# Kernel optimization log

Hardware: AMD Instinct MI355X
Metric: run time of the kernel (lower is better)

The kernel has to match this reference:

```python
import jax, jax.numpy as jnp
import numpy as np

B, N_IN, N_LATENT, STEPS = 256, 1024, 128, 256


def setup_inputs() -> dict:
    key = jax.random.key(0)
    kx, kf, kt = jax.random.split(key, 3)
    x = jax.random.normal(kx, (B, N_IN), dtype=jnp.float32)
    # transform ~ N(0, 0.1) per module's initialize_weights
    transform = 0.1 * jax.random.normal(kf, (N_IN, N_LATENT), dtype=jnp.float32)
    # transition scaled so spectral radius ~0.9 (std*sqrt(n_latent) ~ 0.9)
    # to keep the 256-step linear recurrence numerically stable
    transition = (0.9 / np.sqrt(N_LATENT)) * jax.random.normal(
        kt, (N_LATENT, N_LATENT), dtype=jnp.float32)
    return {"x": x, "transform": transform, "transition": transition,
            "steps": STEPS}


def reference(x, transform, transition, steps):
    # x: [B, n_in] -> latent0: [B, n_latent]
    latent0 = x @ transform

    def step(lat, _):
        lat = lat @ transition  # [B, n_latent]
        return lat, lat

    # lats: [steps, B, n_latent] -- latent states AFTER each transition
    _, lats = jax.lax.scan(step, latent0, None, length=steps)
    # project all latent states back to data space in one contraction
    # out[b, n, s] = sum_l lats[s, b, l] * transform[n, l]
    out = jnp.einsum('sbl,nl->bns', lats, transform)  # [B, n_in, steps]
    return out
```

## Files before the change

### kernel.cpp

```cpp
#include <hip/hip_runtime.h>
#include <hip/hip_bf16.h>

#define NIN 1024
#define NL 128
#define CMS 32768
#define MAGIC 0x4D474331

typedef __attribute__((ext_vector_type(8))) short bf16x8_t;
typedef __attribute__((ext_vector_type(4))) float f32x4_t;

__device__ inline unsigned short f2bf(float f) {
    __hip_bfloat16 h = __float2bfloat16(f);
    return *reinterpret_cast<unsigned short*>(&h);
}
__device__ inline float bf2f(unsigned short u) {
    unsigned int x = (unsigned int)u << 16;
    return __uint_as_float(x);
}
__device__ inline ushort4 pack4(f32x4_t v) {
    ushort4 o;
    o.x = f2bf(v[0]); o.y = f2bf(v[1]); o.z = f2bf(v[2]); o.w = f2bf(v[3]);
    return o;
}

__device__ __forceinline__ void stageBT(const float* __restrict__ Bg,
                                        unsigned short* BtHi, unsigned short* BtLo) {
    int t = threadIdx.x;
    for (int idx = t; idx < 4096; idx += 256) {
        int l = idx >> 5, c4 = (idx & 31) * 4;
        f32x4_t v = *(const f32x4_t*)&Bg[(size_t)l * 128 + c4];
#pragma unroll
        for (int q = 0; q < 4; ++q) {
            int c = c4 + q;
            float f = v[q];
            unsigned short hi = f2bf(f);
            unsigned short lo = f2bf(f - bf2f(hi));
            int byt = c * 256 + ((2 * l) ^ ((c & 7) << 4));
            *(unsigned short*)((char*)BtHi + byt) = hi;
            *(unsigned short*)((char*)BtLo + byt) = lo;
        }
    }
}

__device__ __forceinline__ void stageBT_T(const float* __restrict__ Btr,
                                          unsigned short* BtHi, unsigned short* BtLo) {
    int t = threadIdx.x;
    for (int idx = t; idx < 4096; idx += 256) {
        int c = idx >> 5, l4 = (idx & 31) * 4;
        f32x4_t v = *(const f32x4_t*)&Btr[(size_t)c * 128 + l4];
        ushort4 hi, lo;
        hi.x = f2bf(v[0]); lo.x = f2bf(v[0] - bf2f(hi.x));
        hi.y = f2bf(v[1]); lo.y = f2bf(v[1] - bf2f(hi.y));
        hi.z = f2bf(v[2]); lo.z = f2bf(v[2] - bf2f(hi.z));
        hi.w = f2bf(v[3]); lo.w = f2bf(v[3] - bf2f(hi.w));
        int byt = c * 256 + ((2 * l4) ^ ((c & 7) << 4));
        *(ushort4*)((char*)BtHi + byt) = hi;
        *(ushort4*)((char*)BtLo + byt) = lo;
    }
}

__device__ __forceinline__ void loadX(const float* __restrict__ Ag, float* X) {
    int t = threadIdx.x;
    for (int idx = t; idx < 1024; idx += 256) {
        int rr = idx >> 5, c4 = (idx & 31) * 4;
        f32x4_t v = *(const f32x4_t*)&Ag[(size_t)rr * 128 + c4];
        *(f32x4_t*)((char*)X + rr * 512 + ((c4 * 4) ^ ((rr & 7) << 4))) = v;
    }
}

__device__ __forceinline__ void chainStage(const float* X, float* Xn,
                                           const unsigned short* BtHi,
                                           const unsigned short* BtLo) {
    int t = threadIdx.x, w = t >> 6, lane = t & 63;
    int r = lane & 15, g = lane >> 4;
    int rt = w & 1, ctb = (w >> 1) * 4;
    int rr = rt * 16 + r;
    int sw = (rr & 7) << 4;
    bf16x8_t avHi[4], avLo[4];
#pragma unroll
    for (int kk = 0; kk < 4; ++kk) {
        int c0 = (kk * 4 + g) * 8;
        f32x4_t x0 = *(const f32x4_t*)((const char*)X + rr * 512 + ((c0 * 4) ^ sw));
        f32x4_t x1 = *(const f32x4_t*)((const char*)X + rr * 512 + (((c0 + 4) * 4) ^ sw));
        bf16x8_t hi, lo;
#pragma unroll
        for (int q = 0; q < 4; ++q) {
            unsigned short h0 = f2bf(x0[q]);
            hi[q] = (short)h0;
            lo[q] = (short)f2bf(x0[q] - bf2f(h0));
            unsigned short h1 = f2bf(x1[q]);
            hi[4 + q] = (short)h1;
            lo[4 + q] = (short)f2bf(x1[q] - bf2f(h1));
        }
        avHi[kk] = hi; avLo[kk] = lo;
    }
#pragma unroll
    for (int ct = 0; ct < 4; ++ct) {
        int cb = (ctb + ct) * 16 + r;
        int swb = (cb & 7) << 4;
        f32x4_t acc = (f32x4_t){0.f, 0.f, 0.f, 0.f};
#pragma unroll
        for (int kk = 0; kk < 4; ++kk) {
            int lb2 = (kk * 4 + g) * 16;
            int byt = cb * 256 + (lb2 ^ swb);
            bf16x8_t bh = *(const bf16x8_t*)((const char*)BtHi + byt);
            bf16x8_t bl = *(const bf16x8_t*)((const char*)BtLo + byt);
            acc = __builtin_amdgcn_mfma_f32_16x16x32_bf16(bh, avHi[kk], acc, 0, 0, 0);
            acc = __builtin_amdgcn_mfma_f32_16x16x32_bf16(bh, avLo[kk], acc, 0, 0, 0);
            acc = __builtin_amdgcn_mfma_f32_16x16x32_bf16(bl, avHi[kk], acc, 0, 0, 0);
        }
        int cc = (ctb + ct) * 16 + g * 4;
        *(f32x4_t*)((char*)Xn + rr * 512 + ((cc * 4) ^ sw)) = acc;
    }
}

__device__ __forceinline__ void writeXf(const float* X, float* __restrict__ Df) {
    int t = threadIdx.x;
    for (int idx = t; idx < 1024; idx += 256) {
        int rr = idx >> 5, c4 = (idx & 31) * 4;
        f32x4_t v = *(const f32x4_t*)((const char*)X + rr * 512 + ((c4 * 4) ^ ((rr & 7) << 4)));
        *(f32x4_t*)&Df[(size_t)rr * 128 + c4] = v;
    }
}

__device__ __forceinline__ void writeXbf(const float* X,
                                         unsigned short* __restrict__ base, int rstride) {
    int t = threadIdx.x;
    for (int idx = t; idx < 1024; idx += 256) {
        int rr = idx >> 5, c4 = (idx & 31) * 4;
        f32x4_t v = *(const f32x4_t*)((const char*)X + rr * 512 + ((c4 * 4) ^ ((rr & 7) << 4)));
        *(ushort4*)&base[(size_t)rr * rstride + c4] = pack4(v);
    }
}

__device__ __forceinline__ void signal(int* cells, int ci) {
    __syncthreads();
    if (threadIdx.x == 0)
        __hip_atomic_store(&cells[ci], MAGIC, __ATOMIC_RELEASE,
                           __HIP_MEMORY_SCOPE_AGENT);
}
__device__ __forceinline__ void waitRange(int* cells, int c0, int n) {
    for (int q = 0; q < n; ++q) {
        for (int it = 0; it < (1 << 22); ++it) {
            if (__hip_atomic_load(&cells[c0 + q], __ATOMIC_ACQUIRE,
                                  __HIP_MEMORY_SCOPE_AGENT) == MAGIC)
                break;
            __builtin_amdgcn_s_sleep(2);
        }
    }
}

__global__ __launch_bounds__(256) void k_pre(const float* __restrict__ x,
                                             const float* __restrict__ tf,
                                             const float* __restrict__ tr,
                                             float* __restrict__ T4f,
                                             float* __restrict__ T16f,
                                             float* __restrict__ T32f,
                                             float* __restrict__ Cf,
                                             float* __restrict__ Cf1,
                                             unsigned short* __restrict__ Cc,
                                             unsigned short* __restrict__ H,
                                             int* __restrict__ cells) {
    __shared__ __align__(16) char lds[98304];
    unsigned short* BtHi = (unsigned short*)lds;
    unsigned short* BtLo = (unsigned short*)(lds + 32768);
    float* X0 = (float*)(lds + 65536);
    float* X1 = (float*)(lds + 65536 + 16384);
    int blk = blockIdx.x, t = threadIdx.x;

    if (blk < 32) {
        float* xr = (float*)lds;
        int b0 = blk * 8;
        for (int idx = t; idx < 2048; idx += 256) {
            int rr = idx >> 8, c = idx & 255;
            ((float4*)xr)[rr * 256 + c] =
                ((const float4*)(x + (size_t)(b0 + rr) * NIN))[c];
        }
        __syncthreads();
        int cg = t & 31, rs = t >> 5;
        const float* xp = xr + rs * NIN;
        f32x4_t acc = (f32x4_t){0.f, 0.f, 0.f, 0.f};
#pragma unroll 8
        for (int i = 0; i < NIN; ++i) {
            f32x4_t tv = *(const f32x4_t*)&tf[i * NL + cg * 4];
            acc += xp[i] * tv;
        }
        int row = b0 + rs;
        *(f32x4_t*)&Cf[(size_t)row * NL + cg * 4] = acc;
        *(ushort4*)&Cc[(size_t)row * NL + cg * 4] = pack4(acc);
        signal(cells, blk);
    } else if (blk < 36) {
        int r0 = (blk - 32) * 32;
        stageBT(tr, BtHi, BtLo);
        loadX(tr + (size_t)r0 * NL, X0);
        __syncthreads();
        float* cur = X0; float* nxt = X1;
        for (int s = 0; s < 3; ++s) {
            chainStage(cur, nxt, BtHi, BtLo);
            __syncthreads();
            float* tmp = cur; cur = nxt; nxt = tmp;
        }
        writeXf(cur, T4f + (size_t)r0 * NL);
        signal(cells, blk);
    } else if (blk < 40) {
        int i = blk - 36, r0 = i * 32;
        if (t == 0) { waitRange(cells, 32, 4); __threadfence(); }
        __syncthreads();
        stageBT(T4f, BtHi, BtLo);
        loadX(T4f + (size_t)r0 * NL, X0);
        __syncthreads();
        float* cur = X0; float* nxt = X1;
        for (int s = 1; s <= 7; ++s) {
            chainStage(cur, nxt, BtHi, BtLo);
            __syncthreads();
            if (s == 3) {
                writeXf(nxt, T16f + (size_t)r0 * NL);
                signal(cells, 36 + i);
            }
            if (s == 7) {
                writeXf(nxt, T32f + (size_t)r0 * NL);
                signal(cells, 40 + i);
            }
            float* tmp = cur; cur = nxt; nxt = tmp;
        }
    } else if (blk < 48) {
        int cb = blk - 40, r0 = cb * 32;
        if (t == 0) {
            waitRange(cells, 36, 4);
            waitRange(cells, cb * 4, 4);
            __threadfence();
        }
        __syncthreads();
        stageBT(T16f, BtHi, BtLo);
        loadX(Cf + (size_t)r0 * NL, X0);
        __syncthreads();
        chainStage(X0, X1, BtHi, BtLo);
        __syncthreads();
        writeXf(X1, Cf1 + (size_t)r0 * NL);
        writeXbf(X1, Cc + (size_t)CMS + (size_t)r0 * NL, NL);
        signal(cells, 44 + cb);
    } else if (blk < 56) {
        int cb = blk - 48, r0 = cb * 32;
        if (t == 0) {
            waitRange(cells, 40, 4);
            waitRange(cells, cb * 4, 4);
            __threadfence();
        }
        __syncthreads();
        stageBT(T32f, BtHi, BtLo);
        loadX(Cf + (size_t)r0 * NL, X0);
        __syncthreads();
        float* cur = X0; float* nxt = X1;
        for (int k = 1; k <= 7; ++k) {
            chainStage(cur, nxt, BtHi, BtLo);
            __syncthreads();
            writeXbf(nxt, Cc + (size_t)(2 * k) * CMS + (size_t)r0 * NL, NL);
            float* tmp = cur; cur = nxt; nxt = tmp;
        }
    } else if (blk < 64) {
        int cb = blk - 56, r0 = cb * 32;
        if (t == 0) {
            waitRange(cells, 40, 4);
            waitRange(cells, 44 + cb, 1);
            __threadfence();
        }
        __syncthreads();
        stageBT(T32f, BtHi, BtLo);
        loadX(Cf1 + (size_t)r0 * NL, X0);
        __syncthreads();
        float* cur = X0; float* nxt = X1;
        for (int k = 1; k <= 7; ++k) {
            chainStage(cur, nxt, BtHi, BtLo);
            __syncthreads();
            writeXbf(nxt, Cc + (size_t)(1 + 2 * k) * CMS + (size_t)r0 * NL, NL);
            float* tmp = cur; cur = nxt; nxt = tmp;
        }
    } else {
        int n0 = (blk - 64) * 32;
        stageBT_T(tr, BtHi, BtLo);
        loadX(tf + (size_t)n0 * NL, X0);
        __syncthreads();
        float* cur = X0; float* nxt = X1;
        for (int s = 1; s <= 16; ++s) {
            chainStage(cur, nxt, BtHi, BtLo);
            __syncthreads();
            writeXbf(nxt, H + ((size_t)n0 * 16 + (s - 1)) * NL, 16 * NL);
            float* tmp = cur; cur = nxt; nxt = tmp;
        }
    }
}

__global__ __launch_bounds__(256) void k_main(const unsigned short* __restrict__ Cc,
                                              const unsigned short* __restrict__ H,
                                              float* __restrict__ out) {
    int bid = blockIdx.x;
    int e = ((bid & 7) << 7) | (bid >> 3);
    int ct = e >> 3, bt = (e >> 2) & 1, jq = e & 3;
    __shared__ __align__(16) char lds[49152];
    char* lB = lds;
    int t = threadIdx.x;
    const unsigned short* Bg = H + (size_t)(ct * 128) * NL;
    for (int i = t; i < 2048; i += 256) {
        int row = i >> 4, c = i & 15;
        int sw = (c * 16) ^ ((row & 7) << 4);
        *(bf16x8_t*)(lB + row * 256 + sw) =
            *(const bf16x8_t*)(Bg + (size_t)row * NL + c * 8);
    }
    __syncthreads();
    int w = t >> 6, lane = t & 63;
    int wr = (w >> 1) * 64;
    int wc = (w & 1) * 64;
    int r = lane & 15, g = lane >> 4;
    char* slab = lds + 32768 + w * 4096;

    for (int mf = 0; mf < 4; ++mf) {
        int brow_base = bt * 128 + wr + mf * 16;
        bf16x8_t av[4][4];
#pragma unroll
        for (int jj4 = 0; jj4 < 4; ++jj4) {
            int j = jq * 4 + jj4;
            const unsigned short* Arow =
                Cc + (size_t)j * CMS + (size_t)(brow_base + r) * NL;
#pragma unroll
            for (int kk = 0; kk < 4; ++kk)
                av[jj4][kk] = *(const bf16x8_t*)(Arow + (kk * 4 + g) * 8);
        }
        for (int nf = 0; nf < 4; ++nf) {
            int nn = (w & 1) * 4 + nf;
            int rowB = wc + nf * 16 + r;
            bf16x8_t bvv[4];
#pragma unroll
            for (int kk = 0; kk < 4; ++kk)
                bvv[kk] = *(const bf16x8_t*)(
                    lB + rowB * 256 + (((kk * 4 + g) * 16) ^ ((rowB & 7) << 4)));
            f32x4_t acc4[4];
#pragma unroll
            for (int q = 0; q < 4; ++q) acc4[q] = (f32x4_t){0.f, 0.f, 0.f, 0.f};
#pragma unroll
            for (int jj4 = 0; jj4 < 4; ++jj4)
#pragma unroll
                for (int kk = 0; kk < 4; ++kk)
                    acc4[jj4] = __builtin_amdgcn_mfma_f32_16x16x32_bf16(
                        bvv[kk], av[jj4][kk], acc4[jj4], 0, 0, 0);
#pragma unroll
            for (int jj4 = 0; jj4 < 4; ++jj4) {
                int boff = r * 256 + ((jj4 * 64 + g * 16 + r * 32) & 255);
                *(f32x4_t*)(slab + boff) = acc4[jj4];
            }
#pragma unroll
            for (int i2 = 0; i2 < 4; ++i2) {
                int lin = i2 * 1024 + lane * 16;
                int rs = lin >> 8, cb = lin & 255;
                f32x4_t v = *(const f32x4_t*)(slab + rs * 256 + ((cb + rs * 32) & 255));
                size_t o = (size_t)(brow_base + rs) * (NIN * 256) +
                           (size_t)(ct * 8 + nn) * 256 + jq * 64 + (cb >> 2);
                *(f32x4_t*)&out[o] = v;
            }
        }
    }
}

extern "C" void kernel_launch(void* const* d_in, const int* in_sizes, int n_in,
                              void* d_out, int out_size, void* d_ws, size_t ws_size,
                              hipStream_t stream) {
    const float* x = (const float*)d_in[0];
    const float* tf = (const float*)d_in[1];
    const float* tr = (const float*)d_in[2];
    float* out = (float*)d_out;

    float* T4f = (float*)d_ws;
    float* T16f = T4f + 16384;
    float* T32f = T16f + 16384;
    float* Cf = T32f + 16384;
    float* Cf1 = Cf + (size_t)256 * NL;
    unsigned short* Cc = (unsigned short*)(Cf1 + (size_t)256 * NL);
    unsigned short* H = Cc + (size_t)16 * CMS;
    int* cells = (int*)(H + (size_t)16384 * NL);

    k_pre<<<96, 256, 0, stream>>>(x, tf, tr, T4f, T16f, T32f, Cf, Cf1, Cc, H, cells);
    k_main<<<1024, 256, 0, stream>>>(Cc, H, out);
}
```

Before: 105.8 us.

## Fuse precompute and main GEMM into one persistent launch with flag waits

Merges the two launches into one 1120-block kernel of 512 threads. The first 96 blocks run the precompute chains, using only 256 active threads in the chain stages, and each publishes a completion flag. The remaining 1024 output blocks spin on all 96 flags before doing the projection GEMM with 8 waves each. The goal is to remove the second kernel launch and the gap between launches. In exchange it risks deadlock or stalls if waiting blocks occupy CUs before producer blocks are scheduled, and the larger 98KB LDS allocation lowers occupancy for the main phase.

```diff
diff --git a/kernel.cpp b/kernel.cpp
--- a/kernel.cpp
+++ b/kernel.cpp
@@ -26,7 +26,7 @@
 __device__ __forceinline__ void stageBT(const float* __restrict__ Bg,
                                         unsigned short* BtHi, unsigned short* BtLo) {
     int t = threadIdx.x;
-    for (int idx = t; idx < 4096; idx += 256) {
+    for (int idx = t; idx < 4096; idx += 512) {
         int l = idx >> 5, c4 = (idx & 31) * 4;
         f32x4_t v = *(const f32x4_t*)&Bg[(size_t)l * 128 + c4];
 #pragma unroll
@@ -45,7 +45,7 @@
 __device__ __forceinline__ void stageBT_T(const float* __restrict__ Btr,
                                           unsigned short* BtHi, unsigned short* BtLo) {
     int t = threadIdx.x;
-    for (int idx = t; idx < 4096; idx += 256) {
+    for (int idx = t; idx < 4096; idx += 512) {
         int c = idx >> 5, l4 = (idx & 31) * 4;
         f32x4_t v = *(const f32x4_t*)&Btr[(size_t)c * 128 + l4];
         ushort4 hi, lo;
@@ -61,7 +61,7 @@
 
 __device__ __forceinline__ void loadX(const float* __restrict__ Ag, float* X) {
     int t = threadIdx.x;
-    for (int idx = t; idx < 1024; idx += 256) {
+    for (int idx = t; idx < 1024; idx += 512) {
         int rr = idx >> 5, c4 = (idx & 31) * 4;
         f32x4_t v = *(const f32x4_t*)&Ag[(size_t)rr * 128 + c4];
         *(f32x4_t*)((char*)X + rr * 512 + ((c4 * 4) ^ ((rr & 7) << 4))) = v;
@@ -71,7 +71,9 @@
 __device__ __forceinline__ void chainStage(const float* X, float* Xn,
                                            const unsigned short* BtHi,
                                            const unsigned short* BtLo) {
-    int t = threadIdx.x, w = t >> 6, lane = t & 63;
+    int t = threadIdx.x;
+    if (t >= 256) return;
+    int w = t >> 6, lane = t & 63;
     int r = lane & 15, g = lane >> 4;
     int rt = w & 1, ctb = (w >> 1) * 4;
     int rr = rt * 16 + r;
@@ -116,7 +118,7 @@
 
 __device__ __forceinline__ void writeXf(const float* X, float* __restrict__ Df) {
     int t = threadIdx.x;
-    for (int idx = t; idx < 1024; idx += 256) {
+    for (int idx = t; idx < 1024; idx += 512) {
         int rr = idx >> 5, c4 = (idx & 31) * 4;
         f32x4_t v = *(const f32x4_t*)((const char*)X + rr * 512 + ((c4 * 4) ^ ((rr & 7) << 4)));
         *(f32x4_t*)&Df[(size_t)rr * 128 + c4] = v;
@@ -126,18 +128,16 @@
 __device__ __forceinline__ void writeXbf(const float* X,
                                          unsigned short* __restrict__ base, int rstride) {
     int t = threadIdx.x;
-    for (int idx = t; idx < 1024; idx += 256) {
+    for (int idx = t; idx < 1024; idx += 512) {
         int rr = idx >> 5, c4 = (idx & 31) * 4;
         f32x4_t v = *(const f32x4_t*)((const char*)X + rr * 512 + ((c4 * 4) ^ ((rr & 7) << 4)));
         *(ushort4*)&base[(size_t)rr * rstride + c4] = pack4(v);
     }
 }
 
-__device__ __forceinline__ void signal(int* cells, int ci) {
-    __syncthreads();
-    if (threadIdx.x == 0)
-        __hip_atomic_store(&cells[ci], MAGIC, __ATOMIC_RELEASE,
-                           __HIP_MEMORY_SCOPE_AGENT);
+__device__ __forceinline__ void relCell(int* cells, int ci) {
+    __hip_atomic_store(&cells[ci], MAGIC, __ATOMIC_RELEASE,
+                       __HIP_MEMORY_SCOPE_AGENT);
 }
 __device__ __forceinline__ void waitRange(int* cells, int c0, int n) {
     for (int q = 0; q < n; ++q) {
@@ -150,7 +150,7 @@
     }
 }
 
-__global__ __launch_bounds__(256) void k_pre(const float* __restrict__ x,
+__global__ __launch_bounds__(512) void k_all(const float* __restrict__ x,
                                              const float* __restrict__ tf,
                                              const float* __restrict__ tr,
                                              float* __restrict__ T4f,
@@ -160,7 +160,8 @@
                                              float* __restrict__ Cf1,
                                              unsigned short* __restrict__ Cc,
                                              unsigned short* __restrict__ H,
-                                             int* __restrict__ cells) {
+                                             int* __restrict__ cells,
+                                             float* __restrict__ out) {
     __shared__ __align__(16) char lds[98304];
     unsigned short* BtHi = (unsigned short*)lds;
     unsigned short* BtLo = (unsigned short*)(lds + 32768);
@@ -168,153 +169,175 @@
     float* X1 = (float*)(lds + 65536 + 16384);
     int blk = blockIdx.x, t = threadIdx.x;
 
-    if (blk < 32) {
-        float* xr = (float*)lds;
-        int b0 = blk * 8;
-        for (int idx = t; idx < 2048; idx += 256) {
-            int rr = idx >> 8, c = idx & 255;
-            ((float4*)xr)[rr * 256 + c] =
-                ((const float4*)(x + (size_t)(b0 + rr) * NIN))[c];
-        }
-        __syncthreads();
-        int cg = t & 31, rs = t >> 5;
-        const float* xp = xr + rs * NIN;
-        f32x4_t acc = (f32x4_t){0.f, 0.f, 0.f, 0.f};
+    if (blk < 96) {
+        if (blk < 32) {
+            float* xr = (float*)lds;
+            int b0 = blk * 8;
+            for (int idx = t; idx < 2048; idx += 512) {
+                int rr = idx >> 8, c = idx & 255;
+                ((float4*)xr)[rr * 256 + c] =
+                    ((const float4*)(x + (size_t)(b0 + rr) * NIN))[c];
+            }
+            __syncthreads();
+            if (t < 256) {
+                int cg = t & 31, rs = t >> 5;
+                const float* xp = xr + rs * NIN;
+                f32x4_t acc = (f32x4_t){0.f, 0.f, 0.f, 0.f};
 #pragma unroll 8
-        for (int i = 0; i < NIN; ++i) {
-            f32x4_t tv = *(const f32x4_t*)&tf[i * NL + cg * 4];
-            acc += xp[i] * tv;
-        }
-        int row = b0 + rs;
-        *(f32x4_t*)&Cf[(size_t)row * NL + cg * 4] = acc;
-        *(ushort4*)&Cc[(size_t)row * NL + cg * 4] = pack4(acc);
-        signal(cells, blk);
-    } else if (blk < 36) {
-        int r0 = (blk - 32) * 32;
-        stageBT(tr, BtHi, BtLo);
-        loadX(tr + (size_t)r0 * NL, X0);
-        __syncthreads();
-        float* cur = X0; float* nxt = X1;
-        for (int s = 0; s < 3; ++s) {
-            chainStage(cur, nxt, BtHi, BtLo);
-            __syncthreads();
-            float* tmp = cur; cur = nxt; nxt = tmp;
-        }
-        writeXf(cur, T4f + (size_t)r0 * NL);
-        signal(cells, blk);
-    } else if (blk < 40) {
-        int i = blk - 36, r0 = i * 32;
-        if (t == 0) { waitRange(cells, 32, 4); __threadfence(); }
-        __syncthreads();
-        stageBT(T4f, BtHi, BtLo);
-        loadX(T4f + (size_t)r0 * NL, X0);
-        __syncthreads();
-        float* cur = X0; float* nxt = X1;
-        for (int s = 1; s <= 7; ++s) {
-            chainStage(cur, nxt, BtHi, BtLo);
-            __syncthreads();
-            if (s == 3) {
-                writeXf(nxt, T16f + (size_t)r0 * NL);
-                signal(cells, 36 + i);
-            }
-            if (s == 7) {
-                writeXf(nxt, T32f + (size_t)r0 * NL);
-                signal(cells, 40 + i);
-            }
-            float* tmp = cur; cur = nxt; nxt = tmp;
-        }
-    } else if (blk < 48) {
-        int cb = blk - 40, r0 = cb * 32;
-        if (t == 0) {
-            waitRange(cells, 36, 4);
-            waitRange(cells, cb * 4, 4);
-            __threadfence();
-        }
-        __syncthreads();
-        stageBT(T16f, BtHi, BtLo);
-        loadX(Cf + (size_t)r0 * NL, X0);
-        __syncthreads();
-        chainStage(X0, X1, BtHi, BtLo);
-        __syncthreads();
-        writeXf(X1, Cf1 + (size_t)r0 * NL);
-        writeXbf(X1, Cc + (size_t)CMS + (size_t)r0 * NL, NL);
-        signal(cells, 44 + cb);
-    } else if (blk < 56) {
-        int cb = blk - 48, r0 = cb * 32;
-        if (t == 0) {
-            waitRange(cells, 40, 4);
-            waitRange(cells, cb * 4, 4);
-            __threadfence();
-        }
-        __syncthreads();
-        stageBT(T32f, BtHi, BtLo);
-        loadX(Cf + (size_t)r0 * NL, X0);
-        __syncthreads();
-        float* cur = X0; float* nxt = X1;
-        for (int k = 1; k <= 7; ++k) {
-            chainStage(cur, nxt, BtHi, BtLo);
-            __syncthreads();
-            writeXbf(nxt, Cc + (size_t)(2 * k) * CMS + (size_t)r0 * NL, NL);
-            float* tmp = cur; cur = nxt; nxt = tmp;
-        }
-    } else if (blk < 64) {
-        int cb = blk - 56, r0 = cb * 32;
-        if (t == 0) {
-            waitRange(cells, 40, 4);
-            waitRange(cells, 44 + cb, 1);
-            __threadfence();
-        }
-        __syncthreads();
-        stageBT(T32f, BtHi, BtLo);
-        loadX(Cf1 + (size_t)r0 * NL, X0);
-        __syncthreads();
-        float* cur = X0; float* nxt = X1;
-        for (int k = 1; k <= 7; ++k) {
-            chainStage(cur, nxt, BtHi, BtLo);
-            __syncthreads();
-            writeXbf(nxt, Cc + (size_t)(1 + 2 * k) * CMS + (size_t)r0 * NL, NL);
-            float* tmp = cur; cur = nxt; nxt = tmp;
-        }
-    } else {
-        int n0 = (blk - 64) * 32;
-        stageBT_T(tr, BtHi, BtLo);
-        loadX(tf + (size_t)n0 * NL, X0);
-        __syncthreads();
-        float* cur = X0; float* nxt = X1;
-        for (int s = 1; s <= 16; ++s) {
-            chainStage(cur, nxt, BtHi, BtLo);
-            __syncthreads();
-            writeXbf(nxt, H + ((size_t)n0 * 16 + (s - 1)) * NL, 16 * NL);
-            float* tmp = cur; cur = nxt; nxt = tmp;
-        }
-    }
-}
-
-__global__ __launch_bounds__(256) void k_main(const unsigned short* __restrict__ Cc,
-                                              const unsigned short* __restrict__ H,
-                                              float* __restrict__ out) {
-    int bid = blockIdx.x;
+                for (int i = 0; i < NIN; ++i) {
+                    f32x4_t tv = *(const f32x4_t*)&tf[i * NL + cg * 4];
+                    acc += xp[i] * tv;
+                }
+                int row = b0 + rs;
+                *(f32x4_t*)&Cf[(size_t)row * NL + cg * 4] = acc;
+                *(ushort4*)&Cc[(size_t)row * NL + cg * 4] = pack4(acc);
+            }
+            __syncthreads();
+            if (t == 0) { relCell(cells, blk); relCell(cells, 64 + blk); }
+        } else if (blk < 36) {
+            int r0 = (blk - 32) * 32;
+            stageBT(tr, BtHi, BtLo);
+            loadX(tr + (size_t)r0 * NL, X0);
+            __syncthreads();
+            float* cur = X0; float* nxt = X1;
+            for (int s = 0; s < 3; ++s) {
+                chainStage(cur, nxt, BtHi, BtLo);
+                __syncthreads();
+                float* tmp = cur; cur = nxt; nxt = tmp;
+            }
+            writeXf(cur, T4f + (size_t)r0 * NL);
+            __syncthreads();
+            if (t == 0) { relCell(cells, blk); relCell(cells, 64 + blk); }
+        } else if (blk < 40) {
+            int i = blk - 36, r0 = i * 32;
+            if (t == 0) { waitRange(cells, 32, 4); __threadfence(); }
+            __syncthreads();
+            stageBT(T4f, BtHi, BtLo);
+            loadX(T4f + (size_t)r0 * NL, X0);
+            __syncthreads();
+            float* cur = X0; float* nxt = X1;
+            for (int s = 1; s <= 7; ++s) {
+                chainStage(cur, nxt, BtHi, BtLo);
+                __syncthreads();
+                if (s == 3) {
+                    writeXf(nxt, T16f + (size_t)r0 * NL);
+                    __syncthreads();
+                    if (t == 0) relCell(cells, 36 + i);
+                }
+                if (s == 7) {
+                    writeXf(nxt, T32f + (size_t)r0 * NL);
+                    __syncthreads();
+                    if (t == 0) { relCell(cells, 40 + i); relCell(cells, 64 + blk); }
+                }
+                float* tmp = cur; cur = nxt; nxt = tmp;
+            }
+        } else if (blk < 48) {
+            int cb = blk - 40, r0 = cb * 32;
+            if (t == 0) {
+                waitRange(cells, 36, 4);
+                waitRange(cells, cb * 4, 4);
+                __threadfence();
+            }
+            __syncthreads();
+            stageBT(T16f, BtHi, BtLo);
+            loadX(Cf + (size_t)r0 * NL, X0);
+            __syncthreads();
+            chainStage(X0, X1, BtHi, BtLo);
+            __syncthreads();
+            writeXf(X1, Cf1 + (size_t)r0 * NL);
+            writeXbf(X1, Cc + (size_t)CMS + (size_t)r0 * NL, NL);
+            __syncthreads();
+            if (t == 0) { relCell(cells, 44 + cb); relCell(cells, 64 + blk); }
+        } else if (blk < 56) {
+            int cb = blk - 48, r0 = cb * 32;
+            if (t == 0) {
+                waitRange(cells, 40, 4);
+                waitRange(cells, cb * 4, 4);
+                __threadfence();
+            }
+            __syncthreads();
+            stageBT(T32f, BtHi, BtLo);
+            loadX(Cf + (size_t)r0 * NL, X0);
+            __syncthreads();
+            float* cur = X0; float* nxt = X1;
+            for (int k = 1; k <= 7; ++k) {
+                chainStage(cur, nxt, BtHi, BtLo);
+                __syncthreads();
+                writeXbf(nxt, Cc + (size_t)(2 * k) * CMS + (size_t)r0 * NL, NL);
+                float* tmp = cur; cur = nxt; nxt = tmp;
+            }
+            __syncthreads();
+            if (t == 0) relCell(cells, 64 + blk);
+        } else if (blk < 64) {
+            int cb = blk - 56, r0 = cb * 32;
+            if (t == 0) {
+                waitRange(cells, 40, 4);
+                waitRange(cells, 44 + cb, 1);
+                __threadfence();
+            }
+            __syncthreads();
+            stageBT(T32f, BtHi, BtLo);
+            loadX(Cf1 + (size_t)r0 * NL, X0);
+            __syncthreads();
+            float* cur = X0; float* nxt = X1;
+            for (int k = 1; k <= 7; ++k) {
+                chainStage(cur, nxt, BtHi, BtLo);
+                __syncthreads();
+                writeXbf(nxt, Cc + (size_t)(1 + 2 * k) * CMS + (size_t)r0 * NL, NL);
+                float* tmp = cur; cur = nxt; nxt = tmp;
+            }
+            __syncthreads();
+            if (t == 0) relCell(cells, 64 + blk);
+        } else {
+            int n0 = (blk - 64) * 32;
+            stageBT_T(tr, BtHi, BtLo);
+            loadX(tf + (size_t)n0 * NL, X0);
+            __syncthreads();
+            float* cur = X0; float* nxt = X1;
+            for (int s = 1; s <= 16; ++s) {
+                chainStage(cur, nxt, BtHi, BtLo);
+                __syncthreads();
+                writeXbf(nxt, H + ((size_t)n0 * 16 + (s - 1)) * NL, 16 * NL);
+                float* tmp = cur; cur = nxt; nxt = tmp;
+            }
+            __syncthreads();
+            if (t == 0) relCell(cells, 64 + blk);
+        }
+        return;
+    }
+
+    if (t < 96) {
+        for (int it = 0; it < (1 << 22); ++it) {
+            if (__hip_atomic_load(&cells[64 + t], __ATOMIC_ACQUIRE,
+                                  __HIP_MEMORY_SCOPE_AGENT) == MAGIC)
+                break;
+            __builtin_amdgcn_s_sleep(2);
+        }
+    }
+    __syncthreads();
+    if (t == 0) __threadfence();
+    __syncthreads();
+
+    int bid = blk - 96;
     int e = ((bid & 7) << 7) | (bid >> 3);
     int ct = e >> 3, bt = (e >> 2) & 1, jq = e & 3;
-    __shared__ __align__(16) char lds[49152];
     char* lB = lds;
-    int t = threadIdx.x;
     const unsigned short* Bg = H + (size_t)(ct * 128) * NL;
-    for (int i = t; i < 2048; i += 256) {
+    for (int i = t; i < 2048; i += 512) {
         int row = i >> 4, c = i & 15;
         int sw = (c * 16) ^ ((row & 7) << 4);
         *(bf16x8_t*)(lB + row * 256 + sw) =
             *(const bf16x8_t*)(Bg + (size_t)row * NL + c * 8);
     }
     __syncthreads();
-    int w = t >> 6, lane = t & 63;
-    int wr = (w >> 1) * 64;
-    int wc = (w & 1) * 64;
+    int lane = t & 63, w = t >> 6;
+    int rowgrp = w >> 1, colh = w & 1;
     int r = lane & 15, g = lane >> 4;
+    int wc = colh * 64;
     char* slab = lds + 32768 + w * 4096;
 
-    for (int mf = 0; mf < 4; ++mf) {
-        int brow_base = bt * 128 + wr + mf * 16;
+    for (int mf = 0; mf < 2; ++mf) {
+        int brow_base = bt * 128 + rowgrp * 32 + mf * 16;
         bf16x8_t av[4][4];
 #pragma unroll
         for (int jj4 = 0; jj4 < 4; ++jj4) {
@@ -326,7 +349,7 @@
                 av[jj4][kk] = *(const bf16x8_t*)(Arow + (kk * 4 + g) * 8);
         }
         for (int nf = 0; nf < 4; ++nf) {
-            int nn = (w & 1) * 4 + nf;
+            int nn = colh * 4 + nf;
             int rowB = wc + nf * 16 + r;
             bf16x8_t bvv[4];
 #pragma unroll
@@ -377,6 +400,6 @@
     unsigned short* H = Cc + (size_t)16 * CMS;
     int* cells = (int*)(H + (size_t)16384 * NL);
 
-    k_pre<<<96, 256, 0, stream>>>(x, tf, tr, T4f, T16f, T32f, Cf, Cf1, Cc, H, cells);
-    k_main<<<1024, 256, 0, stream>>>(Cc, H, out);
-}
+    k_all<<<1120, 512, 0, stream>>>(x, tf, tr, T4f, T16f, T32f, Cf, Cf1,
+                                    Cc, H, cells, out);
+}
```

Measured after the change: 420.0 us. +296.9%, slower.
